# Performance work log

Measured on AMD Instinct MI355X. Metric: run time of the kernel, lower is better.

## Reference

```python
import jax, jax.numpy as jnp
import numpy as np
from jax import lax

NUM_DISP = 64
BLOCK = 21
EPS = 1e-12  # F.normalize default eps


def _box_sum(v):
    # v: (N, H, W) -> BLOCK x BLOCK zero-padded box sum (same shape), separable.
    p = BLOCK // 2
    v = v[:, None]  # (N,1,H,W)
    kv = jnp.ones((1, 1, BLOCK, 1), v.dtype)
    kh = jnp.ones((1, 1, 1, BLOCK), v.dtype)
    v = lax.conv_general_dilated(v, kv, (1, 1), ((p, p), (0, 0)))
    v = lax.conv_general_dilated(v, kh, (1, 1), ((0, 0), (p, p)))
    return v[:, 0]


def _l2norm_c(img):
    n = jnp.sqrt(jnp.sum(img * img, axis=1, keepdims=True))
    return img / jnp.maximum(n, EPS)


def _disparity(left, right):
    # left, right: (B, 3, H, W)
    left = _l2norm_c(left)
    right = _l2norm_c(right)
    B, C, H, W = left.shape
    d = jnp.arange(NUM_DISP)
    xs = jnp.arange(W)
    idx = xs[None, :] - d[:, None]              # (D, W): source column in right image
    valid = (idx >= 0)
    r_shift = right[:, :, :, jnp.clip(idx, 0)]  # (B, C, H, D, W)
    r_shift = jnp.where(valid[None, None, None], r_shift, 0.0)
    # per-pixel channel-summed absolute difference -> (B, D, H, W)
    diff = jnp.sum(jnp.abs(left[:, :, :, None, :] - r_shift), axis=1)  # (B, H, D, W)
    diff = jnp.transpose(diff, (0, 2, 1, 3))    # (B, D, H, W)
    cost = _box_sum(diff.reshape(B * NUM_DISP, H, W)).reshape(B, NUM_DISP, H, W)
    cost = cost / (C * BLOCK * BLOCK)           # mean SAD over block elements
    return jnp.argmin(cost, axis=1).astype(left.dtype)  # (B, H, W)


def setup_inputs() -> dict:
    key = jax.random.key(0)
    k1, k2 = jax.random.split(key)
    x = jax.random.normal(k1, (2, 6, 320, 512), dtype=jnp.float32)
    gt = jax.random.normal(k2, (2, 6, 320, 512), dtype=jnp.float32)
    return {"x": x, "gt": gt}


def reference(x, gt):
    disp_gt = _disparity(gt[:, :3], gt[:, 3:])
    disp_pred = _disparity(x[:, :3], x[:, 3:])
    return jnp.mean(jnp.abs(disp_pred - disp_gt))
```

## Files before the change

kernel.cpp:

```cpp
#include <hip/hip_runtime.h>
#include <math.h>

constexpr int B = 2, H = 320, W = 512, D = 64;
constexpr int HW = H * W;
constexpr int R = 10;
constexpr int SEG = 80;
constexpr int NSEG = H / SEG;
constexpr int RS = 540;
constexpr float EPS = 1e-12f;

__global__ void k_norm(const float* __restrict__ x, const float* __restrict__ gt,
                       float4* __restrict__ nrm4) {
    int idx = blockIdx.x * blockDim.x + threadIdx.x;
    if (idx >= 2 * B * HW) return;
    int t = idx / (B * HW);
    int rem = idx - t * (B * HW);
    int b = rem / HW;
    int hw = rem - b * HW;
    const float* p = (t == 0 ? x : gt) + (size_t)b * 6 * HW + hw;
    float v0 = p[0],      v1 = p[HW],     v2 = p[2 * HW];
    float v3 = p[3 * HW], v4 = p[4 * HW], v5 = p[5 * HW];
    float n1 = fmaxf(sqrtf(v0 * v0 + v1 * v1 + v2 * v2), EPS);
    float n2 = fmaxf(sqrtf(v3 * v3 + v4 * v4 + v5 * v5), EPS);
    float4* q = nrm4 + (size_t)(t * B + b) * 2 * HW + hw;
    q[0]  = make_float4(v0 / n1, v1 / n1, v2 / n1, 0.f);
    q[HW] = make_float4(v3 / n2, v4 / n2, v5 / n2, 0.f);
}

__global__ __launch_bounds__(512, 4) void k_cost(const float4* __restrict__ nrm4,
                                                 float* __restrict__ cost, int t) {
    int blk = blockIdx.x;
    int combo = blk & 7;
    int d = blk >> 3;
    int b = combo >> 2;
    int seg = combo & 3;
    int w = threadIdx.x;
    const float4* L4 = nrm4 + (size_t)(t * B + b) * 2 * HW;
    const float4* R4 = L4 + HW;
    const bool val = (w >= d);
    const int wr = val ? (w - d) : 0;
    const int h0 = seg * SEG;

    __shared__ float ring[21][W];
    __shared__ float vsbuf[8][RS];

    {
        int j = w >> 6, k = w & 63;
        if (k < 10) vsbuf[j][k] = 0.f;
        else if (k < 28) vsbuf[j][522 + (k - 10)] = 0.f;
    }

    auto diff = [&](int h) -> float {
        float4 l = L4[(size_t)h * W + w];
        if (val) {
            float4 r = R4[(size_t)h * W + wr];
            return fabsf(l.x - r.x) + fabsf(l.y - r.y) + fabsf(l.z - r.z);
        }
        return fabsf(l.x) + fabsf(l.y) + fabsf(l.z);
    };

    float vs = 0.f;
    for (int k = 0; k < 20; ++k) {
        int h = h0 - R + k;
        float dv = (h >= 0) ? diff(h) : 0.f;
        ring[k][w] = dv;
        vs += dv;
    }
    ring[20][w] = 0.f;

    float* cp = cost + ((size_t)(b * D + d) * H) * W;
    const int cc = threadIdx.x >> 3;
    const int jj = threadIdx.x & 7;

    for (int ss = 0; ss < SEG / 8; ++ss) {
#pragma unroll
        for (int j = 0; j < 8; ++j) {
            int i = ss * 8 + j;
            int slot = (i + 20) % 21;
            int hn = h0 + i + R;
            float dv = (hn < H) ? diff(hn) : 0.f;
            float dold = ring[slot][w];
            ring[slot][w] = dv;
            vs += dv - dold;
            vsbuf[j][10 + w] = vs;
        }
        __syncthreads();
        {
            const float* vp = &vsbuf[jj][8 * cc];
            float wnd[28];
#pragma unroll
            for (int q = 0; q < 7; ++q) {
                float4 v4 = *(const float4*)(vp + 4 * q);
                wnd[4 * q] = v4.x; wnd[4 * q + 1] = v4.y;
                wnd[4 * q + 2] = v4.z; wnd[4 * q + 3] = v4.w;
            }
            float o = 0.f;
#pragma unroll
            for (int k = 0; k < 21; ++k) o += wnd[k];
            float out[8];
            out[0] = o;
#pragma unroll
            for (int k = 1; k < 8; ++k) { o += wnd[20 + k] - wnd[k - 1]; out[k] = o; }
            float* op = cp + (size_t)(h0 + ss * 8 + jj) * W + 8 * cc;
            *(float4*)(op)     = make_float4(out[0], out[1], out[2], out[3]);
            *(float4*)(op + 4) = make_float4(out[4], out[5], out[6], out[7]);
        }
        __syncthreads();
    }
}

__global__ void k_argmin(const float* __restrict__ cost, float* __restrict__ disp) {
    int idx = blockIdx.x * 256 + threadIdx.x;
    if (idx >= B * (HW / 4)) return;
    int b = idx / (HW / 4);
    int g = idx - b * (HW / 4);
    const float4* cp = (const float4*)cost + (size_t)b * D * (HW / 4) + g;
    float4 v0 = cp[0];
    float bb[4] = {v0.x, v0.y, v0.z, v0.w};
    int bd[4] = {0, 0, 0, 0};
#pragma unroll 4
    for (int d = 1; d < D; ++d) {
        float4 v = cp[(size_t)d * (HW / 4)];
        if (v.x < bb[0]) { bb[0] = v.x; bd[0] = d; }
        if (v.y < bb[1]) { bb[1] = v.y; bd[1] = d; }
        if (v.z < bb[2]) { bb[2] = v.z; bd[2] = d; }
        if (v.w < bb[3]) { bb[3] = v.w; bd[3] = d; }
    }
    ((float4*)disp)[idx] = make_float4((float)bd[0], (float)bd[1], (float)bd[2], (float)bd[3]);
}

__global__ void k_red1(const float* __restrict__ a, const float* __restrict__ b2,
                       float* __restrict__ part, int n) {
    __shared__ float sm[256];
    int tid = threadIdx.x;
    float s = 0.f;
    for (int i = blockIdx.x * 256 + tid; i < n; i += gridDim.x * 256)
        s += fabsf(a[i] - b2[i]);
    sm[tid] = s;
    __syncthreads();
    for (int off = 128; off; off >>= 1) {
        if (tid < off) sm[tid] += sm[tid + off];
        __syncthreads();
    }
    if (!tid) part[blockIdx.x] = sm[0];
}

__global__ void k_red2(const float* __restrict__ part, float* __restrict__ out,
                       int nb, float inv) {
    __shared__ float sm[256];
    int tid = threadIdx.x;
    float s = 0.f;
    for (int i = tid; i < nb; i += 256) s += part[i];
    sm[tid] = s;
    __syncthreads();
    for (int off = 128; off; off >>= 1) {
        if (tid < off) sm[tid] += sm[tid + off];
        __syncthreads();
    }
    if (!tid) out[0] = sm[0] * inv;
}

extern "C" void kernel_launch(void* const* d_in, const int* in_sizes, int n_in,
                              void* d_out, int out_size, void* d_ws, size_t ws_size,
                              hipStream_t stream) {
    const float* x  = (const float*)d_in[0];
    const float* gt = (const float*)d_in[1];

    float4* nrm4 = (float4*)d_ws;
    float* cost  = (float*)(nrm4 + (size_t)2 * B * 2 * HW);
    float* disp  = cost + (size_t)B * D * HW;
    float* part  = disp + (size_t)2 * B * HW;

    k_norm<<<(2 * B * HW + 255) / 256, 256, 0, stream>>>(x, gt, nrm4);

    for (int t = 0; t < 2; ++t) {
        k_cost<<<B * NSEG * D, 512, 0, stream>>>(nrm4, cost, t);
        k_argmin<<<(B * (HW / 4) + 255) / 256, 256, 0, stream>>>(cost, disp + (size_t)t * B * HW);
    }

    constexpr int NB = 640;
    k_red1<<<NB, 256, 0, stream>>>(disp, disp + (size_t)B * HW, part, B * HW);
    k_red2<<<1, 256, 0, stream>>>(part, (float*)d_out, NB, 1.f / (float)(B * HW));
}
```

Baseline: 203.9 us.

## Double-buffer box-sum staging, batch ring loads, fuse argmin with abs-diff reduction

The cost kernel double-buffers the horizontal-sum shared buffer so one barrier per 8-row step can be dropped. It also batches the ring-buffer reads and the global diff loads ahead of the writes, and lowers launch bounds to 2 blocks per CU so more registers are available. The argmin kernels now process scalar pixels instead of float4, and the second argmin fuses the abs-difference and block reduction, which removes the separate reduction pass. Shared memory use grows with the double buffer, and occupancy may drop.

```diff
diff --git a/kernel.cpp b/kernel.cpp
--- a/kernel.cpp
+++ b/kernel.cpp
@@ -6,7 +6,7 @@
 constexpr int R = 10;
 constexpr int SEG = 80;
 constexpr int NSEG = H / SEG;
-constexpr int RS = 540;
+constexpr int RS = 548;
 constexpr float EPS = 1e-12f;
 
 __global__ void k_norm(const float* __restrict__ x, const float* __restrict__ gt,
@@ -27,7 +27,7 @@
     q[HW] = make_float4(v3 / n2, v4 / n2, v5 / n2, 0.f);
 }
 
-__global__ __launch_bounds__(512, 4) void k_cost(const float4* __restrict__ nrm4,
+__global__ __launch_bounds__(512, 2) void k_cost(const float4* __restrict__ nrm4,
                                                  float* __restrict__ cost, int t) {
     int blk = blockIdx.x;
     int combo = blk & 7;
@@ -42,12 +42,12 @@
     const int h0 = seg * SEG;
 
     __shared__ float ring[21][W];
-    __shared__ float vsbuf[8][RS];
+    __shared__ float vsb[2][8][RS];
 
     {
         int j = w >> 6, k = w & 63;
-        if (k < 10) vsbuf[j][k] = 0.f;
-        else if (k < 28) vsbuf[j][522 + (k - 10)] = 0.f;
+        if (k < 10)      { vsb[0][j][k] = 0.f;       vsb[1][j][k] = 0.f; }
+        else if (k < 20) { vsb[0][j][512 + k] = 0.f; vsb[1][j][512 + k] = 0.f; }
     }
 
     auto diff = [&](int h) -> float {
@@ -62,9 +62,9 @@
     float vs = 0.f;
     for (int k = 0; k < 20; ++k) {
         int h = h0 - R + k;
-        float dv = (h >= 0) ? diff(h) : 0.f;
-        ring[k][w] = dv;
-        vs += dv;
+        float dv0 = (h >= 0) ? diff(h) : 0.f;
+        ring[k][w] = dv0;
+        vs += dv0;
     }
     ring[20][w] = 0.f;
 
@@ -72,77 +72,84 @@
     const int cc = threadIdx.x >> 3;
     const int jj = threadIdx.x & 7;
 
+    int slot0 = 20;
     for (int ss = 0; ss < SEG / 8; ++ss) {
+        int sl[8];
+        float dold[8], dv[8];
+#pragma unroll
+        for (int j = 0; j < 8; ++j) { int s2 = slot0 + j; if (s2 >= 21) s2 -= 21; sl[j] = s2; }
+#pragma unroll
+        for (int j = 0; j < 8; ++j) dold[j] = ring[sl[j]][w];
 #pragma unroll
         for (int j = 0; j < 8; ++j) {
-            int i = ss * 8 + j;
-            int slot = (i + 20) % 21;
-            int hn = h0 + i + R;
-            float dv = (hn < H) ? diff(hn) : 0.f;
-            float dold = ring[slot][w];
-            ring[slot][w] = dv;
-            vs += dv - dold;
-            vsbuf[j][10 + w] = vs;
+            int hn = h0 + ss * 8 + j + R;
+            dv[j] = (hn < H) ? diff(hn) : 0.f;
         }
+#pragma unroll
+        for (int j = 0; j < 8; ++j) ring[sl[j]][w] = dv[j];
+        float* vrow = &vsb[ss & 1][0][0];
+#pragma unroll
+        for (int j = 0; j < 8; ++j) { vs += dv[j] - dold[j]; vrow[j * RS + 10 + w] = vs; }
         __syncthreads();
-        {
-            const float* vp = &vsbuf[jj][8 * cc];
-            float wnd[28];
+        const float* vp = &vsb[ss & 1][jj][8 * cc];
+        float wnd[28];
 #pragma unroll
-            for (int q = 0; q < 7; ++q) {
-                float4 v4 = *(const float4*)(vp + 4 * q);
-                wnd[4 * q] = v4.x; wnd[4 * q + 1] = v4.y;
-                wnd[4 * q + 2] = v4.z; wnd[4 * q + 3] = v4.w;
-            }
-            float o = 0.f;
+        for (int q = 0; q < 7; ++q) {
+            float4 v4 = *(const float4*)(vp + 4 * q);
+            wnd[4 * q] = v4.x; wnd[4 * q + 1] = v4.y;
+            wnd[4 * q + 2] = v4.z; wnd[4 * q + 3] = v4.w;
+        }
+        float o = 0.f;
 #pragma unroll
-            for (int k = 0; k < 21; ++k) o += wnd[k];
-            float out[8];
-            out[0] = o;
+        for (int k = 0; k < 21; ++k) o += wnd[k];
+        float out[8];
+        out[0] = o;
 #pragma unroll
-            for (int k = 1; k < 8; ++k) { o += wnd[20 + k] - wnd[k - 1]; out[k] = o; }
-            float* op = cp + (size_t)(h0 + ss * 8 + jj) * W + 8 * cc;
-            *(float4*)(op)     = make_float4(out[0], out[1], out[2], out[3]);
-            *(float4*)(op + 4) = make_float4(out[4], out[5], out[6], out[7]);
-        }
-        __syncthreads();
+        for (int k = 1; k < 8; ++k) { o += wnd[20 + k] - wnd[k - 1]; out[k] = o; }
+        float* op = cp + (size_t)(h0 + ss * 8 + jj) * W + 8 * cc;
+        *(float4*)(op)     = make_float4(out[0], out[1], out[2], out[3]);
+        *(float4*)(op + 4) = make_float4(out[4], out[5], out[6], out[7]);
+        slot0 += 8; if (slot0 >= 21) slot0 -= 21;
     }
 }
 
-__global__ void k_argmin(const float* __restrict__ cost, float* __restrict__ disp) {
+__global__ void k_argmin0(const float* __restrict__ cost, float* __restrict__ disp) {
     int idx = blockIdx.x * 256 + threadIdx.x;
-    if (idx >= B * (HW / 4)) return;
-    int b = idx / (HW / 4);
-    int g = idx - b * (HW / 4);
-    const float4* cp = (const float4*)cost + (size_t)b * D * (HW / 4) + g;
-    float4 v0 = cp[0];
-    float bb[4] = {v0.x, v0.y, v0.z, v0.w};
-    int bd[4] = {0, 0, 0, 0};
-#pragma unroll 4
+    if (idx >= B * HW) return;
+    int b = idx / HW, hw = idx - b * HW;
+    const float* cp = cost + (size_t)b * D * HW + hw;
+    float best = cp[0]; int bd = 0;
+#pragma unroll 16
     for (int d = 1; d < D; ++d) {
-        float4 v = cp[(size_t)d * (HW / 4)];
-        if (v.x < bb[0]) { bb[0] = v.x; bd[0] = d; }
-        if (v.y < bb[1]) { bb[1] = v.y; bd[1] = d; }
-        if (v.z < bb[2]) { bb[2] = v.z; bd[2] = d; }
-        if (v.w < bb[3]) { bb[3] = v.w; bd[3] = d; }
+        float v = cp[(size_t)d * HW];
+        if (v < best) { best = v; bd = d; }
     }
-    ((float4*)disp)[idx] = make_float4((float)bd[0], (float)bd[1], (float)bd[2], (float)bd[3]);
+    disp[idx] = (float)bd;
 }
 
-__global__ void k_red1(const float* __restrict__ a, const float* __restrict__ b2,
-                       float* __restrict__ part, int n) {
+__global__ void k_argmin1(const float* __restrict__ cost, const float* __restrict__ disp0,
+                          float* __restrict__ part) {
+    int idx = blockIdx.x * 256 + threadIdx.x;
+    float s = 0.f;
+    if (idx < B * HW) {
+        int b = idx / HW, hw = idx - b * HW;
+        const float* cp = cost + (size_t)b * D * HW + hw;
+        float best = cp[0]; int bd = 0;
+#pragma unroll 16
+        for (int d = 1; d < D; ++d) {
+            float v = cp[(size_t)d * HW];
+            if (v < best) { best = v; bd = d; }
+        }
+        s = fabsf((float)bd - disp0[idx]);
+    }
     __shared__ float sm[256];
-    int tid = threadIdx.x;
-    float s = 0.f;
-    for (int i = blockIdx.x * 256 + tid; i < n; i += gridDim.x * 256)
-        s += fabsf(a[i] - b2[i]);
-    sm[tid] = s;
+    sm[threadIdx.x] = s;
     __syncthreads();
     for (int off = 128; off; off >>= 1) {
-        if (tid < off) sm[tid] += sm[tid + off];
+        if (threadIdx.x < off) sm[threadIdx.x] += sm[threadIdx.x + off];
         __syncthreads();
     }
-    if (!tid) part[blockIdx.x] = sm[0];
+    if (!threadIdx.x) part[blockIdx.x] = sm[0];
 }
 
 __global__ void k_red2(const float* __restrict__ part, float* __restrict__ out,
@@ -171,14 +178,14 @@
     float* disp  = cost + (size_t)B * D * HW;
     float* part  = disp + (size_t)2 * B * HW;
 
+    constexpr int NPIX_BLKS = (B * HW + 255) / 256;
+
     k_norm<<<(2 * B * HW + 255) / 256, 256, 0, stream>>>(x, gt, nrm4);
 
-    for (int t = 0; t < 2; ++t) {
-        k_cost<<<B * NSEG * D, 512, 0, stream>>>(nrm4, cost, t);
-        k_argmin<<<(B * (HW / 4) + 255) / 256, 256, 0, stream>>>(cost, disp + (size_t)t * B * HW);
-    }
+    k_cost<<<B * NSEG * D, 512, 0, stream>>>(nrm4, cost, 0);
+    k_argmin0<<<NPIX_BLKS, 256, 0, stream>>>(cost, disp);
+    k_cost<<<B * NSEG * D, 512, 0, stream>>>(nrm4, cost, 1);
+    k_argmin1<<<NPIX_BLKS, 256, 0, stream>>>(cost, disp, part);
 
-    constexpr int NB = 640;
-    k_red1<<<NB, 256, 0, stream>>>(disp, disp + (size_t)B * HW, part, B * HW);
-    k_red2<<<1, 256, 0, stream>>>(part, (float*)d_out, NB, 1.f / (float)(B * HW));
+    k_red2<<<1, 256, 0, stream>>>(part, (float*)d_out, NPIX_BLKS, 1.f / (float)(B * HW));
 }
```

Result: no change. 205.1 us (+0.6%).
